# Kernel optimization log

Hardware: AMD Instinct MI355X
Metric: run time of the kernel (lower is better)

The kernel has to match this reference:

```python
import jax, jax.numpy as jnp
import numpy as np

N_GRAPHS = 512


def setup_inputs() -> dict:
    key = jax.random.key(0)
    ks = jax.random.split(key, 9)
    N, E, V, NE, D, C = 100000, 500000, 50000, 1000000, 300, 20
    nodes_batch = jax.random.randint(ks[0], (N,), 0, V)
    edges_batch = jax.random.randint(ks[1], (E,), 0, NE)
    src = jax.random.randint(ks[2], (E,), 0, N)
    dst = jax.random.randint(ks[3], (E,), 0, N)
    graph_ids = jnp.sort(jax.random.randint(ks[4], (N,), 0, N_GRAPHS))
    node_embed = jax.random.normal(ks[5], (V, D), dtype=jnp.float32)
    edge_embed = jax.random.uniform(ks[6], (NE, 1), dtype=jnp.float32)
    fc_w = jax.random.normal(ks[7], (D, C), dtype=jnp.float32) * 0.05
    fc_b = jnp.zeros((C,), dtype=jnp.float32)
    return {"nodes_batch": nodes_batch, "edges_batch": edges_batch, "src": src,
            "dst": dst, "graph_ids": graph_ids, "node_embed": node_embed,
            "edge_embed": edge_embed, "fc_w": fc_w, "fc_b": fc_b}


def reference(nodes_batch, edges_batch, src, dst, graph_ids, node_embed, edge_embed, fc_w, fc_b):
    N = nodes_batch.shape[0]
    h = node_embed[nodes_batch]                      # [N, D] node features
    w = edge_embed[edges_batch]                      # [E, 1] scalar edge weights
    msg = h[src] * w                                 # [E, D] src_mul_edge
    # DGL mean reduce over incoming edges; nodes with no in-edges get 0.
    summed = jax.ops.segment_sum(msg, dst, num_segments=N)
    cnt = jax.ops.segment_sum(jnp.ones((msg.shape[0],), msg.dtype), dst, num_segments=N)
    h_new = summed / jnp.maximum(cnt, 1.0)[:, None]  # [N, D]
    g = jax.ops.segment_sum(h_new, graph_ids, num_segments=N_GRAPHS)  # sum_nodes readout
    out = jax.nn.relu(g) @ fc_w + fc_b               # dropout is identity at eval
    return out
```

## Files before the change

### kernel.cpp

```cpp
#include <hip/hip_runtime.h>
#include <hip/hip_bf16.h>

#define NG 512
#define D_DIM 300
#define C_DIM 20
#define NSLICE 8
#define NBINS (NSLICE * NG)
#define GSTRIDE 304
#define SC_EPB 2048

static __device__ inline ushort f2bf(float f) {
    union { float f; unsigned u; } x; x.f = f;
    unsigned r = x.u + 0x7FFF + ((x.u >> 16) & 1);
    return (ushort)(r >> 16);
}

__global__ __launch_bounds__(256) void convert_b(const float* __restrict__ B,
                                                 ushort* __restrict__ B16, int K) {
    int total = K * 38;
    for (int idx = blockIdx.x * 256 + threadIdx.x; idx < total; idx += gridDim.x * 256) {
        int row = idx / 38;
        int k = idx - row * 38;
        int d0 = k * 8;
        const float* p = B + (size_t)row * D_DIM + d0;
        float f0, f1, f2, f3, f4, f5, f6, f7;
        if (d0 + 8 <= D_DIM) {
            float4 a = *(const float4*)p;
            float4 b = *(const float4*)(p + 4);
            f0 = a.x; f1 = a.y; f2 = a.z; f3 = a.w;
            f4 = b.x; f5 = b.y; f6 = b.z; f7 = b.w;
        } else {
            float4 a = *(const float4*)p;
            f0 = a.x; f1 = a.y; f2 = a.z; f3 = a.w;
            f4 = f5 = f6 = f7 = 0.f;
        }
        uint4 pk;
        pk.x = (unsigned)f2bf(f0) | ((unsigned)f2bf(f1) << 16);
        pk.y = (unsigned)f2bf(f2) | ((unsigned)f2bf(f3) << 16);
        pk.z = (unsigned)f2bf(f4) | ((unsigned)f2bf(f5) << 16);
        pk.w = (unsigned)f2bf(f6) | ((unsigned)f2bf(f7) << 16);
        *(uint4*)(B16 + (size_t)row * GSTRIDE + d0) = pk;
    }
}

__global__ __launch_bounds__(1024) void count_hist(const int* __restrict__ dst,
                                                   const int* __restrict__ src,
                                                   const int* __restrict__ nodes_batch,
                                                   const int* __restrict__ graph_ids,
                                                   int* __restrict__ cnt,
                                                   int* __restrict__ kcnt,
                                                   int E, int KS) {
    __shared__ int h[NBINS];
    int t = threadIdx.x;
    for (int i = t; i < NBINS; i += 1024) h[i] = 0;
    __syncthreads();
    for (int e = blockIdx.x * 1024 + t; e < E; e += gridDim.x * 1024) {
        int d = dst[e];
        atomicAdd(&cnt[d], 1);
        int v = nodes_batch[src[e]];
        int g = graph_ids[d];
        atomicAdd(&h[(v / KS) * NG + g], 1);
    }
    __syncthreads();
    for (int i = t; i < NBINS; i += 1024)
        if (h[i]) atomicAdd(&kcnt[i], h[i]);
}

__global__ __launch_bounds__(1024) void scan4k(const int* __restrict__ kcnt,
                                               int* __restrict__ koff,
                                               int* __restrict__ kfill, int E) {
    __shared__ int s[1024];
    int t = threadIdx.x;
    int l0 = kcnt[t * 4 + 0], l1 = kcnt[t * 4 + 1], l2 = kcnt[t * 4 + 2], l3 = kcnt[t * 4 + 3];
    int sum = l0 + l1 + l2 + l3;
    s[t] = sum;
    __syncthreads();
    for (int off = 1; off < 1024; off <<= 1) {
        int x = (t >= off) ? s[t - off] : 0;
        __syncthreads();
        s[t] += x;
        __syncthreads();
    }
    int base = s[t] - sum;
    int v0 = base, v1 = base + l0, v2 = base + l0 + l1, v3 = base + l0 + l1 + l2;
    koff[t * 4 + 0] = v0; kfill[t * 4 + 0] = v0;
    koff[t * 4 + 1] = v1; kfill[t * 4 + 1] = v1;
    koff[t * 4 + 2] = v2; kfill[t * 4 + 2] = v2;
    koff[t * 4 + 3] = v3; kfill[t * 4 + 3] = v3;
    if (t == 1023) koff[NBINS] = E;
}

__global__ __launch_bounds__(512) void scatter4k(const int* __restrict__ src,
                                                 const int* __restrict__ dst,
                                                 const int* __restrict__ eb,
                                                 const int* __restrict__ nodes_batch,
                                                 const float* __restrict__ edge_embed,
                                                 const int* __restrict__ graph_ids,
                                                 const int* __restrict__ cnt,
                                                 int* __restrict__ kfill,
                                                 int2* __restrict__ elist, int E, int KS) {
    __shared__ int bcnt[NBINS];
    __shared__ int base[NBINS];
    int t = threadIdx.x;
    int e0 = blockIdx.x * SC_EPB;
    for (int i = t; i < NBINS; i += 512) bcnt[i] = 0;
    __syncthreads();
    int vs[SC_EPB / 512];
    float scales[SC_EPB / 512];
    int keys[SC_EPB / 512];
#pragma unroll
    for (int k = 0; k < SC_EPB / 512; k++) {
        int e = e0 + k * 512 + t;
        keys[k] = -1;
        if (e < E) {
            int d = dst[e];
            int v = nodes_batch[src[e]];
            keys[k] = (v / KS) * NG + graph_ids[d];
            vs[k] = v;
            scales[k] = edge_embed[eb[e]] / (float)max(cnt[d], 1);
            atomicAdd(&bcnt[keys[k]], 1);
        }
    }
    __syncthreads();
    for (int i = t; i < NBINS; i += 512) {
        int c = bcnt[i];
        base[i] = c ? atomicAdd(&kfill[i], c) : 0;
        bcnt[i] = 0;
    }
    __syncthreads();
#pragma unroll
    for (int k = 0; k < SC_EPB / 512; k++) {
        if (keys[k] >= 0) {
            int pos = base[keys[k]] + atomicAdd(&bcnt[keys[k]], 1);
            elist[pos] = make_int2(vs[k], __float_as_int(scales[k]));
        }
    }
}

static __device__ inline void acc8(uint4 q, float s, float* a) {
    a[0] += s * __uint_as_float(q.x << 16);
    a[1] += s * __uint_as_float(q.x & 0xFFFF0000u);
    a[2] += s * __uint_as_float(q.y << 16);
    a[3] += s * __uint_as_float(q.y & 0xFFFF0000u);
    a[4] += s * __uint_as_float(q.z << 16);
    a[5] += s * __uint_as_float(q.z & 0xFFFF0000u);
    a[6] += s * __uint_as_float(q.w << 16);
    a[7] += s * __uint_as_float(q.w & 0xFFFF0000u);
}

__global__ __launch_bounds__(256, 4) void accum_wave(const int2* __restrict__ elist,
                                                     const int* __restrict__ koff,
                                                     const ushort* __restrict__ B16,
                                                     float* __restrict__ gslice) {
    int t = threadIdx.x;
    int wv = t >> 6, lane = t & 63;
    if (lane >= 38) return;
    int slice = blockIdx.x & 7;
    int g = ((blockIdx.x >> 3) << 2) + wv;
    int bin = slice * NG + g;
    int beg = koff[bin], end = koff[bin + 1];
    const ushort* Bl = B16 + (lane << 3);

    float a[8] = {0.f, 0.f, 0.f, 0.f, 0.f, 0.f, 0.f, 0.f};
    int j = beg;
    for (; j + 8 <= end; j += 8) {
        int2 p0 = elist[j + 0], p1 = elist[j + 1], p2 = elist[j + 2], p3 = elist[j + 3];
        int2 p4 = elist[j + 4], p5 = elist[j + 5], p6 = elist[j + 6], p7 = elist[j + 7];
        uint4 q0 = *(const uint4*)(Bl + (size_t)p0.x * GSTRIDE);
        uint4 q1 = *(const uint4*)(Bl + (size_t)p1.x * GSTRIDE);
        uint4 q2 = *(const uint4*)(Bl + (size_t)p2.x * GSTRIDE);
        uint4 q3 = *(const uint4*)(Bl + (size_t)p3.x * GSTRIDE);
        uint4 q4 = *(const uint4*)(Bl + (size_t)p4.x * GSTRIDE);
        uint4 q5 = *(const uint4*)(Bl + (size_t)p5.x * GSTRIDE);
        uint4 q6 = *(const uint4*)(Bl + (size_t)p6.x * GSTRIDE);
        uint4 q7 = *(const uint4*)(Bl + (size_t)p7.x * GSTRIDE);
        acc8(q0, __int_as_float(p0.y), a);
        acc8(q1, __int_as_float(p1.y), a);
        acc8(q2, __int_as_float(p2.y), a);
        acc8(q3, __int_as_float(p3.y), a);
        acc8(q4, __int_as_float(p4.y), a);
        acc8(q5, __int_as_float(p5.y), a);
        acc8(q6, __int_as_float(p6.y), a);
        acc8(q7, __int_as_float(p7.y), a);
    }
    for (; j + 4 <= end; j += 4) {
        int2 p0 = elist[j + 0], p1 = elist[j + 1], p2 = elist[j + 2], p3 = elist[j + 3];
        uint4 q0 = *(const uint4*)(Bl + (size_t)p0.x * GSTRIDE);
        uint4 q1 = *(const uint4*)(Bl + (size_t)p1.x * GSTRIDE);
        uint4 q2 = *(const uint4*)(Bl + (size_t)p2.x * GSTRIDE);
        uint4 q3 = *(const uint4*)(Bl + (size_t)p3.x * GSTRIDE);
        acc8(q0, __int_as_float(p0.y), a);
        acc8(q1, __int_as_float(p1.y), a);
        acc8(q2, __int_as_float(p2.y), a);
        acc8(q3, __int_as_float(p3.y), a);
    }
    for (; j < end; ++j) {
        int2 pr = elist[j];
        uint4 q = *(const uint4*)(Bl + (size_t)pr.x * GSTRIDE);
        acc8(q, __int_as_float(pr.y), a);
    }
    float4* outp = (float4*)(gslice + (size_t)bin * GSTRIDE + (lane << 3));
    outp[0] = make_float4(a[0], a[1], a[2], a[3]);
    outp[1] = make_float4(a[4], a[5], a[6], a[7]);
}

__global__ __launch_bounds__(320) void fc_kernel(const float* __restrict__ gslice,
                                                 const float* __restrict__ fc_w,
                                                 const float* __restrict__ fc_b,
                                                 float* __restrict__ out) {
    __shared__ float wlds[D_DIM * C_DIM];
    __shared__ float accs[D_DIM];
    __shared__ float outs[C_DIM];
    int gid = blockIdx.x;
    int t = threadIdx.x;
    for (int i = t; i < D_DIM * C_DIM; i += 320) wlds[i] = fc_w[i];
    if (t < D_DIM) {
        float a = 0.f;
#pragma unroll
        for (int s = 0; s < NSLICE; s++)
            a += gslice[(size_t)(s * NG + gid) * GSTRIDE + t];
        accs[t] = a;
    }
    if (t < C_DIM) outs[t] = fc_b[t];
    __syncthreads();
    if (t < C_DIM * 12) {
        int c = t % C_DIM;
        int ch = t / C_DIM;
        float p = 0.f;
#pragma unroll
        for (int d = ch * 25; d < ch * 25 + 25; d++) {
            float gv = accs[d];
            gv = gv > 0.f ? gv : 0.f;
            p += gv * wlds[d * C_DIM + c];
        }
        atomicAdd(&outs[c], p);
    }
    __syncthreads();
    if (t < C_DIM) out[gid * C_DIM + t] = outs[t];
}

extern "C" void kernel_launch(void* const* d_in, const int* in_sizes, int n_in,
                              void* d_out, int out_size, void* d_ws, size_t ws_size,
                              hipStream_t stream) {
    const int* nodes_batch = (const int*)d_in[0];
    const int* edges_batch = (const int*)d_in[1];
    const int* src = (const int*)d_in[2];
    const int* dst = (const int*)d_in[3];
    const int* graph_ids = (const int*)d_in[4];
    const float* node_embed = (const float*)d_in[5];
    const float* edge_embed = (const float*)d_in[6];
    const float* fc_w = (const float*)d_in[7];
    const float* fc_b = (const float*)d_in[8];
    float* out = (float*)d_out;

    int N = in_sizes[0];
    int E = in_sizes[2];
    int K = in_sizes[5] / D_DIM;
    int KS = (K + NSLICE - 1) / NSLICE;

    char* ws = (char*)d_ws;
    size_t off = 0;
    int* cnt = (int*)(ws + off); off += (size_t)N * 4;
    int* kcnt = (int*)(ws + off); off += (size_t)NBINS * 4;
    int* koff = (int*)(ws + off); off += (size_t)(NBINS + 1) * 4;
    int* kfill = (int*)(ws + off); off += (size_t)NBINS * 4;
    off = (off + 15) & ~(size_t)15;
    ushort* B16 = (ushort*)(ws + off); off += (size_t)K * GSTRIDE * 2;
    float* gslice = (float*)(ws + off); off += (size_t)NBINS * GSTRIDE * 4;
    int2* elist = (int2*)(ws + off); off += (size_t)E * 8;

    if (ws_size >= off) {
        hipMemsetAsync(cnt, 0, (size_t)N * 4, stream);
        hipMemsetAsync(kcnt, 0, (size_t)NBINS * 4, stream);
        convert_b<<<2048, 256, 0, stream>>>(node_embed, B16, K);
        count_hist<<<256, 1024, 0, stream>>>(dst, src, nodes_batch, graph_ids, cnt, kcnt, E, KS);
        scan4k<<<1, 1024, 0, stream>>>(kcnt, koff, kfill, E);
        int nsb = (E + SC_EPB - 1) / SC_EPB;
        scatter4k<<<nsb, 512, 0, stream>>>(src, dst, edges_batch, nodes_batch, edge_embed,
                                           graph_ids, cnt, kfill, elist, E, KS);
        accum_wave<<<8 * (NG / 4), 256, 0, stream>>>(elist, koff, B16, gslice);
        fc_kernel<<<NG, 320, 0, stream>>>(gslice, fc_w, fc_b, out);
    }
}
```

Measured before the change: 117.5 us.

## Fuse bf16 conversion with histogram and split accumulation bins across two waves

Merges the bf16 table conversion and the edge histogram into one launch, using disjoint block ranges so the two independent jobs run concurrently and one launch is saved. Each accumulation bin's edge range is split in half between two waves, doubling the grid and writing partial sums to a second gslice copy. The FC kernel then reduces 16 partials per graph instead of 8. This raises parallelism in the gather stage at the cost of extra workspace and a slightly larger final reduction.

```diff
diff --git a/kernel.cpp b/kernel.cpp
--- a/kernel.cpp
+++ b/kernel.cpp
@@ -8,6 +8,8 @@
 #define NBINS (NSLICE * NG)
 #define GSTRIDE 304
 #define SC_EPB 2048
+#define CONV_BLOCKS 1024
+#define HIST_BLOCKS 512
 
 static __device__ inline ushort f2bf(float f) {
     union { float f; unsigned u; } x; x.f = f;
@@ -15,55 +17,57 @@
     return (ushort)(r >> 16);
 }
 
-__global__ __launch_bounds__(256) void convert_b(const float* __restrict__ B,
-                                                 ushort* __restrict__ B16, int K) {
-    int total = K * 38;
-    for (int idx = blockIdx.x * 256 + threadIdx.x; idx < total; idx += gridDim.x * 256) {
-        int row = idx / 38;
-        int k = idx - row * 38;
-        int d0 = k * 8;
-        const float* p = B + (size_t)row * D_DIM + d0;
-        float f0, f1, f2, f3, f4, f5, f6, f7;
-        if (d0 + 8 <= D_DIM) {
-            float4 a = *(const float4*)p;
-            float4 b = *(const float4*)(p + 4);
-            f0 = a.x; f1 = a.y; f2 = a.z; f3 = a.w;
-            f4 = b.x; f5 = b.y; f6 = b.z; f7 = b.w;
-        } else {
-            float4 a = *(const float4*)p;
-            f0 = a.x; f1 = a.y; f2 = a.z; f3 = a.w;
-            f4 = f5 = f6 = f7 = 0.f;
-        }
-        uint4 pk;
-        pk.x = (unsigned)f2bf(f0) | ((unsigned)f2bf(f1) << 16);
-        pk.y = (unsigned)f2bf(f2) | ((unsigned)f2bf(f3) << 16);
-        pk.z = (unsigned)f2bf(f4) | ((unsigned)f2bf(f5) << 16);
-        pk.w = (unsigned)f2bf(f6) | ((unsigned)f2bf(f7) << 16);
-        *(uint4*)(B16 + (size_t)row * GSTRIDE + d0) = pk;
-    }
-}
-
-__global__ __launch_bounds__(1024) void count_hist(const int* __restrict__ dst,
-                                                   const int* __restrict__ src,
-                                                   const int* __restrict__ nodes_batch,
-                                                   const int* __restrict__ graph_ids,
-                                                   int* __restrict__ cnt,
-                                                   int* __restrict__ kcnt,
-                                                   int E, int KS) {
+__global__ __launch_bounds__(512) void prep_fused(const float* __restrict__ B,
+                                                  ushort* __restrict__ B16, int K,
+                                                  const int* __restrict__ dst,
+                                                  const int* __restrict__ src,
+                                                  const int* __restrict__ nodes_batch,
+                                                  const int* __restrict__ graph_ids,
+                                                  int* __restrict__ cnt,
+                                                  int* __restrict__ kcnt,
+                                                  int E, int KS) {
     __shared__ int h[NBINS];
     int t = threadIdx.x;
-    for (int i = t; i < NBINS; i += 1024) h[i] = 0;
-    __syncthreads();
-    for (int e = blockIdx.x * 1024 + t; e < E; e += gridDim.x * 1024) {
-        int d = dst[e];
-        atomicAdd(&cnt[d], 1);
-        int v = nodes_batch[src[e]];
-        int g = graph_ids[d];
-        atomicAdd(&h[(v / KS) * NG + g], 1);
-    }
-    __syncthreads();
-    for (int i = t; i < NBINS; i += 1024)
-        if (h[i]) atomicAdd(&kcnt[i], h[i]);
+    if (blockIdx.x < CONV_BLOCKS) {
+        int total = K * 38;
+        for (int idx = blockIdx.x * 512 + t; idx < total; idx += CONV_BLOCKS * 512) {
+            int row = idx / 38;
+            int k = idx - row * 38;
+            int d0 = k * 8;
+            const float* p = B + (size_t)row * D_DIM + d0;
+            float f0, f1, f2, f3, f4, f5, f6, f7;
+            if (d0 + 8 <= D_DIM) {
+                float4 a = *(const float4*)p;
+                float4 b = *(const float4*)(p + 4);
+                f0 = a.x; f1 = a.y; f2 = a.z; f3 = a.w;
+                f4 = b.x; f5 = b.y; f6 = b.z; f7 = b.w;
+            } else {
+                float4 a = *(const float4*)p;
+                f0 = a.x; f1 = a.y; f2 = a.z; f3 = a.w;
+                f4 = f5 = f6 = f7 = 0.f;
+            }
+            uint4 pk;
+            pk.x = (unsigned)f2bf(f0) | ((unsigned)f2bf(f1) << 16);
+            pk.y = (unsigned)f2bf(f2) | ((unsigned)f2bf(f3) << 16);
+            pk.z = (unsigned)f2bf(f4) | ((unsigned)f2bf(f5) << 16);
+            pk.w = (unsigned)f2bf(f6) | ((unsigned)f2bf(f7) << 16);
+            *(uint4*)(B16 + (size_t)row * GSTRIDE + d0) = pk;
+        }
+    } else {
+        int b = blockIdx.x - CONV_BLOCKS;
+        for (int i = t; i < NBINS; i += 512) h[i] = 0;
+        __syncthreads();
+        for (int e = b * 512 + t; e < E; e += HIST_BLOCKS * 512) {
+            int d = dst[e];
+            atomicAdd(&cnt[d], 1);
+            int v = nodes_batch[src[e]];
+            int g = graph_ids[d];
+            atomicAdd(&h[(v / KS) * NG + g], 1);
+        }
+        __syncthreads();
+        for (int i = t; i < NBINS; i += 512)
+            if (h[i]) atomicAdd(&kcnt[i], h[i]);
+    }
 }
 
 __global__ __launch_bounds__(1024) void scan4k(const int* __restrict__ kcnt,
@@ -156,9 +160,13 @@
     int wv = t >> 6, lane = t & 63;
     if (lane >= 38) return;
     int slice = blockIdx.x & 7;
-    int g = ((blockIdx.x >> 3) << 2) + wv;
+    int g = ((blockIdx.x >> 3) << 1) + (wv >> 1);
+    int h = wv & 1;
     int bin = slice * NG + g;
-    int beg = koff[bin], end = koff[bin + 1];
+    int b0 = koff[bin], b1 = koff[bin + 1];
+    int mid = (b0 + b1) >> 1;
+    int beg = h ? mid : b0;
+    int end = h ? b1 : mid;
     const ushort* Bl = B16 + (lane << 3);
 
     float a[8] = {0.f, 0.f, 0.f, 0.f, 0.f, 0.f, 0.f, 0.f};
@@ -199,7 +207,7 @@
         uint4 q = *(const uint4*)(Bl + (size_t)pr.x * GSTRIDE);
         acc8(q, __int_as_float(pr.y), a);
     }
-    float4* outp = (float4*)(gslice + (size_t)bin * GSTRIDE + (lane << 3));
+    float4* outp = (float4*)(gslice + (size_t)(h * NBINS + bin) * GSTRIDE + (lane << 3));
     outp[0] = make_float4(a[0], a[1], a[2], a[3]);
     outp[1] = make_float4(a[4], a[5], a[6], a[7]);
 }
@@ -217,8 +225,8 @@
     if (t < D_DIM) {
         float a = 0.f;
 #pragma unroll
-        for (int s = 0; s < NSLICE; s++)
-            a += gslice[(size_t)(s * NG + gid) * GSTRIDE + t];
+        for (int p = 0; p < 2 * NSLICE; p++)
+            a += gslice[(size_t)(p * NG + gid) * GSTRIDE + t];
         accs[t] = a;
     }
     if (t < C_DIM) outs[t] = fc_b[t];
@@ -266,19 +274,19 @@
     int* kfill = (int*)(ws + off); off += (size_t)NBINS * 4;
     off = (off + 15) & ~(size_t)15;
     ushort* B16 = (ushort*)(ws + off); off += (size_t)K * GSTRIDE * 2;
-    float* gslice = (float*)(ws + off); off += (size_t)NBINS * GSTRIDE * 4;
+    float* gslice = (float*)(ws + off); off += (size_t)2 * NBINS * GSTRIDE * 4;
     int2* elist = (int2*)(ws + off); off += (size_t)E * 8;
 
     if (ws_size >= off) {
         hipMemsetAsync(cnt, 0, (size_t)N * 4, stream);
         hipMemsetAsync(kcnt, 0, (size_t)NBINS * 4, stream);
-        convert_b<<<2048, 256, 0, stream>>>(node_embed, B16, K);
-        count_hist<<<256, 1024, 0, stream>>>(dst, src, nodes_batch, graph_ids, cnt, kcnt, E, KS);
+        prep_fused<<<CONV_BLOCKS + HIST_BLOCKS, 512, 0, stream>>>(
+            node_embed, B16, K, dst, src, nodes_batch, graph_ids, cnt, kcnt, E, KS);
         scan4k<<<1, 1024, 0, stream>>>(kcnt, koff, kfill, E);
         int nsb = (E + SC_EPB - 1) / SC_EPB;
         scatter4k<<<nsb, 512, 0, stream>>>(src, dst, edges_batch, nodes_batch, edge_embed,
                                            graph_ids, cnt, kfill, elist, E, KS);
-        accum_wave<<<8 * (NG / 4), 256, 0, stream>>>(elist, koff, B16, gslice);
+        accum_wave<<<8 * (NG / 2), 256, 0, stream>>>(elist, koff, B16, gslice);
         fc_kernel<<<NG, 320, 0, stream>>>(gslice, fc_w, fc_b, out);
     }
 }
```

Result: slower. 120.0 us (+2.1%).
